# Optimization experiments

Hardware: AMD Instinct MI355X
Metric: run time of the kernel (lower is better)

The kernel has to match this reference:

```python
import jax, jax.numpy as jnp
import numpy as np

U, I, R, E, K, D, RD, OUT = 100000, 50000, 5, 100000, 4, 16, 64, 64
KF = 2      # selected factor index (self.k)
TAU = 0.5   # contrastive temperature


def setup_inputs() -> dict:
    key = jax.random.key(0)
    ks = jax.random.split(key, 17)
    inp = {
        'user_h': jax.random.normal(ks[0], (R, U, D), jnp.float32),
        'item_h': jax.random.normal(ks[1], (R, I, D), jnp.float32),
        'user_hsum': jax.random.normal(ks[2], (R, U, K, D), jnp.float32) * 0.25,
        'item_hsum': jax.random.normal(ks[3], (R, I, K, D), jnp.float32) * 0.25,
        'review_feat': jax.random.normal(ks[4], (R, E, K, RD), jnp.float32) * 0.2,
        'prototypes': jax.random.normal(ks[5], (K, RD), jnp.float32) * 0.2,
        'eta': jax.random.normal(ks[6], (R, E), jnp.float32),
        'node_w_fwd': jax.random.normal(ks[7], (R, D, D), jnp.float32) / np.sqrt(D),
        'node_w_rev': jax.random.normal(ks[8], (R, D, D), jnp.float32) / np.sqrt(D),
        'review_w_fwd': jax.random.normal(ks[9], (R, RD, D), jnp.float32) / np.sqrt(RD),
        'review_w_rev': jax.random.normal(ks[10], (R, RD, D), jnp.float32) / np.sqrt(RD),
        'ufc_w': jax.random.normal(ks[11], (D, OUT), jnp.float32) / np.sqrt(D),
        'ufc_b': jnp.zeros((OUT,), jnp.float32),
        'ifc_w': jax.random.normal(ks[12], (D, OUT), jnp.float32) / np.sqrt(D),
        'ifc_b': jnp.zeros((OUT,), jnp.float32),
        'rows': jax.random.randint(ks[13], (R, E), 0, U),
        'cols': jax.random.randint(ks[14], (R, E), 0, I),
    }
    return inp


def _l2n(x):
    return x / jnp.linalg.norm(x, axis=-1, keepdims=True)


def reference(user_h, item_h, user_hsum, item_hsum, review_feat, prototypes, eta,
              node_w_fwd, node_w_rev, review_w_fwd, review_w_rev,
              ufc_w, ufc_b, ifc_w, ifc_b, rows, cols):
    # --- per-rating contrastive edge scores (fwd and rev etypes are symmetric) ---
    ead_list = []
    norm_u = jnp.zeros((U,), user_h.dtype)
    norm_i = jnp.zeros((I,), user_h.dtype)
    for r in range(R):
        row, col = rows[r], cols[r]
        # factor-KF node similarity (L2-normalized feats)
        ru = _l2n(user_h[r])[row]               # [E, D]
        ri = _l2n(item_h[r])[col]               # [E, D]
        sim_k = jnp.sum(ru * ri, -1) / TAU      # [E]
        sim_all = jnp.sum(user_hsum[r][row] * item_hsum[r][col], -1) / TAU  # [E, K]
        exp_sim = jnp.exp(sim_k) / jnp.sum(jnp.exp(sim_all), -1)
        # prototype anchor scores on review features
        rf_k = review_feat[r, :, KF, :]                      # [E, RD]
        ad_k = (rf_k @ prototypes[KF]) / TAU                 # [E]
        ad_all = jnp.sum(review_feat[r] * prototypes, -1) / TAU  # [E, K]
        ead = jnp.exp(ad_k) / jnp.sum(jnp.exp(ad_all), -1)
        # sigmoid-gated combine with per-edge eta
        g = jax.nn.sigmoid(eta[r])
        ead = g * ead + (1.0 - g) * exp_sim
        ead_list.append(ead)
        # scatter-sum normalization; fwd+rev each contribute once, then /2 in torch
        norm_u = norm_u + jax.ops.segment_sum(ead, row, num_segments=U)
        norm_i = norm_i + jax.ops.segment_sum(ead, col, num_segments=I)
    # --- normalized edge weights + weighted message passing (HeteroGraphConv sum) ---
    ufeat = jnp.zeros((U, D), user_h.dtype)
    ifeat = jnp.zeros((I, D), user_h.dtype)
    int_dist = []
    for r in range(R):
        row, col = rows[r], cols[r]
        w = ead_list[r] / jnp.sqrt(norm_u[row] * norm_i[col])  # [E]
        int_dist.append(w[:, None])                            # item-side etype weights
        rf_k = review_feat[r, :, KF, :]
        # user -> item messages
        m_fwd = ((user_h[r] @ node_w_fwd[r])[row] + rf_k @ review_w_fwd[r]) * w[:, None]
        ifeat = ifeat + jax.ops.segment_sum(m_fwd, col, num_segments=I)
        # item -> user messages (rev etype, same review feats and weights)
        m_rev = ((item_h[r] @ node_w_rev[r])[col] + rf_k @ review_w_rev[r]) * w[:, None]
        ufeat = ufeat + jax.ops.segment_sum(m_rev, row, num_segments=U)
    int_dist = jnp.concatenate(int_dist, axis=0)  # [R*E, 1]
    leaky = lambda x: jnp.where(x >= 0, x, 0.1 * x)
    ufeat = leaky(ufeat) @ ufc_w + ufc_b
    ifeat = leaky(ifeat) @ ifc_w + ifc_b
    return ufeat, ifeat, int_dist
```

## Files before the change

kernel.cpp:

```cpp
#include <hip/hip_runtime.h>
#include <cstddef>

#define DEV_INLINE __device__ __forceinline__

constexpr int U_N = 100000;
constexpr int I_N = 50000;
constexpr int R_N = 5;
constexpr int E_N = 100000;
constexpr int K_N = 4;
constexpr int D_N = 16;
constexpr int RD_N = 64;
constexpr int OUT_N = 64;
constexpr int KF_N = 2;
constexpr float INV_TAU = 2.0f;

constexpr int NE_TOT = R_N * E_N;
constexpr int NNODE  = U_N + I_N;
constexpr int NB_SCAN = (NNODE + 255) / 256;

constexpr size_t OFS_CNT    = 0;
constexpr size_t OFS_OFF    = 150000;
constexpr size_t OFS_BSUMS  = 300016;
constexpr size_t OFS_CURSOR = 301040;
constexpr size_t OFS_LIST   = 451040;
constexpr size_t OFS_EAD    = 1451040;
constexpr size_t OFS_NORM   = 1951040;
constexpr size_t OFS_MFWD   = 2101040;
constexpr size_t OFS_MREV   = 10101040;

DEV_INLINE float dot4(float4 a, float4 b) { return a.x*b.x + a.y*b.y + a.z*b.z + a.w*b.w; }
DEV_INLINE void fma4(float4& a, float s, float4 w) { a.x += s*w.x; a.y += s*w.y; a.z += s*w.z; a.w += s*w.w; }
DEV_INLINE float comp(float4 v, int i) { return i == 0 ? v.x : i == 1 ? v.y : i == 2 ? v.z : v.w; }

__global__ __launch_bounds__(256) void count_kernel(
    const int* __restrict__ rows, const int* __restrict__ cols, int* __restrict__ cnt)
{
    const int idx = blockIdx.x * 256 + threadIdx.x;
    if (idx >= NE_TOT) return;
    atomicAdd(cnt + rows[idx], 1);
    atomicAdd(cnt + U_N + cols[idx], 1);
}

__global__ __launch_bounds__(256) void scan1_kernel(
    const int* __restrict__ cnt, int* __restrict__ off, int* __restrict__ bsums)
{
    __shared__ int s[256];
    const int t = threadIdx.x;
    const int i = blockIdx.x * 256 + t;
    const int v = (i < NNODE) ? cnt[i] : 0;
    s[t] = v;
    __syncthreads();
#pragma unroll
    for (int d = 1; d < 256; d <<= 1) {
        const int x = (t >= d) ? s[t - d] : 0;
        __syncthreads();
        s[t] += x;
        __syncthreads();
    }
    if (i < NNODE) off[i] = s[t] - v;
    if (t == 255) bsums[blockIdx.x] = s[255];
}

__global__ __launch_bounds__(1024) void scan2_kernel(int* __restrict__ bsums)
{
    __shared__ int s[1024];
    const int t = threadIdx.x;
    const int v = (t < NB_SCAN) ? bsums[t] : 0;
    s[t] = v;
    __syncthreads();
#pragma unroll
    for (int d = 1; d < 1024; d <<= 1) {
        const int x = (t >= d) ? s[t - d] : 0;
        __syncthreads();
        s[t] += x;
        __syncthreads();
    }
    if (t < NB_SCAN) bsums[t] = s[t] - v;
}

__global__ __launch_bounds__(256) void scan3_kernel(
    int* __restrict__ off, const int* __restrict__ bsums, int* __restrict__ cursor)
{
    const int i = blockIdx.x * 256 + threadIdx.x;
    if (i < NNODE) {
        const int v = off[i] + bsums[i >> 8];
        off[i] = v;
        cursor[i] = v;
    }
    if (i == 0) off[NNODE] = 2 * NE_TOT;
}

__global__ __launch_bounds__(256) void fill_kernel(
    const int* __restrict__ rows, const int* __restrict__ cols,
    int* __restrict__ cursor, int* __restrict__ list)
{
    const int idx = blockIdx.x * 256 + threadIdx.x;
    if (idx >= NE_TOT) return;
    const int p = atomicAdd(cursor + rows[idx], 1);
    list[p] = idx;
    const int q = atomicAdd(cursor + U_N + cols[idx], 1);
    list[q] = idx;
}

__global__ __launch_bounds__(256) void phase1_kernel(
    const float* __restrict__ user_h, const float* __restrict__ item_h,
    const float* __restrict__ user_hsum, const float* __restrict__ item_hsum,
    const float* __restrict__ review_feat, const float* __restrict__ prototypes,
    const float* __restrict__ eta,
    const float* __restrict__ node_w_fwd, const float* __restrict__ node_w_rev,
    const float* __restrict__ review_w_fwd, const float* __restrict__ review_w_rev,
    const int* __restrict__ rows, const int* __restrict__ cols,
    float* __restrict__ ead_ws,
    float* __restrict__ m_fwd, float* __restrict__ m_rev)
{
    __shared__ __align__(16) float proto_s[K_N * RD_N];
    __shared__ __align__(16) float nwf_s[D_N * D_N];
    __shared__ __align__(16) float nwr_s[D_N * D_N];
    __shared__ __align__(16) float rwf_s[RD_N * D_N];
    __shared__ __align__(16) float rwr_s[RD_N * D_N];
    const int tid = threadIdx.x;
    const int r = blockIdx.y;
    proto_s[tid] = prototypes[tid];
    nwf_s[tid] = node_w_fwd[r * D_N * D_N + tid];
    nwr_s[tid] = node_w_rev[r * D_N * D_N + tid];
#pragma unroll
    for (int q = 0; q < 4; ++q) {
        rwf_s[q*256 + tid] = review_w_fwd[r * RD_N * D_N + q*256 + tid];
        rwr_s[q*256 + tid] = review_w_rev[r * RD_N * D_N + q*256 + tid];
    }
    __syncthreads();

    const int e = blockIdx.x * 64 + (tid >> 2);
    const int l = tid & 3;
    if (e >= E_N) return;
    const size_t re = (size_t)r * E_N + e;
    const int row = rows[re];
    const int col = cols[re];

    const float4* uh4 = (const float4*)(user_h + ((size_t)r * U_N + row) * D_N);
    const float4* ih4 = (const float4*)(item_h + ((size_t)r * I_N + col) * D_N);
    const float4 a = uh4[l], b = ih4[l];
    float du = dot4(a, a), di = dot4(b, b), dui = dot4(a, b);
    du  += __shfl_xor(du, 1);  du  += __shfl_xor(du, 2);
    di  += __shfl_xor(di, 1);  di  += __shfl_xor(di, 2);
    dui += __shfl_xor(dui, 1); dui += __shfl_xor(dui, 2);
    const float sim_k = dui / sqrtf(du * di) * INV_TAU;

    const float4* us4 = (const float4*)(user_hsum + ((size_t)r * U_N + row) * (K_N * D_N)) + l * 4;
    const float4* is4 = (const float4*)(item_hsum + ((size_t)r * I_N + col) * (K_N * D_N)) + l * 4;
    float s = 0.f;
#pragma unroll
    for (int q = 0; q < 4; ++q) s += dot4(us4[q], is4[q]);
    float ssum = expf(s * INV_TAU);
    ssum += __shfl_xor(ssum, 1); ssum += __shfl_xor(ssum, 2);
    const float exp_sim = expf(sim_k) / ssum;

    const float4* rf4 = (const float4*)(review_feat + re * (size_t)(K_N * RD_N)) + l * 16;
    const float4* pr4 = (const float4*)proto_s + l * 16;
    float t = 0.f;
#pragma unroll
    for (int q = 0; q < 16; ++q) t += dot4(rf4[q], pr4[q]);
    t *= INV_TAU;
    float adsum = expf(t);
    adsum += __shfl_xor(adsum, 1); adsum += __shfl_xor(adsum, 2);
    const float adk = __shfl(t, KF_N, 4);
    const float ead_rev = expf(adk) / adsum;

    const float g = 1.0f / (1.0f + expf(-eta[re]));
    const float ead = g * ead_rev + (1.0f - g) * exp_sim;
    if (l == 0) ead_ws[re] = ead;

    float4 mf = make_float4(0.f, 0.f, 0.f, 0.f);
    float4 mr = make_float4(0.f, 0.f, 0.f, 0.f);
    const float4* nf4 = (const float4*)nwf_s;
    const float4* nr4 = (const float4*)nwr_s;
#pragma unroll
    for (int jq = 0; jq < 4; ++jq) {
        const float4 uv = uh4[jq];
        const float4 iv = ih4[jq];
#pragma unroll
        for (int jj = 0; jj < 4; ++jj) {
            const int j = jq*4 + jj;
            fma4(mf, comp(uv, jj), nf4[j*4 + l]);
            fma4(mr, comp(iv, jj), nr4[j*4 + l]);
        }
    }
    const float4* rfk4 = (const float4*)(review_feat + re * (size_t)(K_N * RD_N) + KF_N * RD_N);
    const float4* rf4w = (const float4*)rwf_s;
    const float4* rr4w = (const float4*)rwr_s;
#pragma unroll
    for (int jq = 0; jq < 16; ++jq) {
        const float4 v4 = rfk4[jq];
#pragma unroll
        for (int jj = 0; jj < 4; ++jj) {
            const int j = jq*4 + jj;
            fma4(mf, comp(v4, jj), rf4w[j*4 + l]);
            fma4(mr, comp(v4, jj), rr4w[j*4 + l]);
        }
    }
    *((float4*)(m_fwd + re * (size_t)D_N) + l) = mf;
    *((float4*)(m_rev + re * (size_t)D_N) + l) = mr;
}

__global__ __launch_bounds__(256) void norm_kernel(
    const int* __restrict__ off, const int* __restrict__ list,
    const float* __restrict__ ead, float* __restrict__ norm)
{
    const int n = blockIdx.x * 256 + threadIdx.x;
    if (n >= NNODE) return;
    const int p0 = off[n], p1 = off[n + 1];
    float acc = 0.f;
    for (int p = p0; p < p1; ++p) acc += ead[list[p]];
    norm[n] = acc;
}

__global__ __launch_bounds__(256) void wscale_kernel(
    const int* __restrict__ rows, const int* __restrict__ cols,
    const float* __restrict__ ead, const float* __restrict__ norm,
    float* __restrict__ w_out)
{
    const int idx = blockIdx.x * 256 + threadIdx.x;
    if (idx >= NE_TOT) return;
    const float nu = norm[rows[idx]];
    const float ni = norm[U_N + cols[idx]];
    w_out[idx] = ead[idx] / sqrtf(nu * ni);
}

__global__ __launch_bounds__(256) void gatherfc_kernel(
    const int* __restrict__ off, const int* __restrict__ list,
    const float* __restrict__ m_fwd, const float* __restrict__ m_rev,
    const float* __restrict__ w_edge,
    const float* __restrict__ ufc_w, const float* __restrict__ ufc_b,
    const float* __restrict__ ifc_w, const float* __restrict__ ifc_b,
    float* __restrict__ out)
{
    __shared__ __align__(16) float uw_s[D_N * OUT_N];
    __shared__ __align__(16) float iw_s[D_N * OUT_N];
    __shared__ __align__(16) float ub_s[OUT_N];
    __shared__ __align__(16) float ib_s[OUT_N];
    const int tid = threadIdx.x;
#pragma unroll
    for (int q = 0; q < 4; ++q) {
        uw_s[q*256 + tid] = ufc_w[q*256 + tid];
        iw_s[q*256 + tid] = ifc_w[q*256 + tid];
    }
    if (tid < OUT_N) ub_s[tid] = ufc_b[tid];
    else if (tid < 2*OUT_N) ib_s[tid - OUT_N] = ifc_b[tid - OUT_N];
    __syncthreads();

    const int gid = blockIdx.x * 256 + tid;
    const int n = gid >> 2;
    const int l = gid & 3;
    if (n >= NNODE) return;
    const int p0 = off[n], p1 = off[n + 1];
    const bool isU = (n < U_N);
    const float* __restrict__ src = isU ? m_rev : m_fwd;
    float4 acc = make_float4(0.f, 0.f, 0.f, 0.f);
    for (int p = p0; p < p1; ++p) {
        const int e = list[p];
        const float w = w_edge[e];
        const float4 v = *((const float4*)(src + (size_t)e * D_N) + l);
        fma4(acc, w, v);
    }
    acc.x = (acc.x >= 0.f) ? acc.x : 0.1f * acc.x;
    acc.y = (acc.y >= 0.f) ? acc.y : 0.1f * acc.y;
    acc.z = (acc.z >= 0.f) ? acc.z : 0.1f * acc.z;
    acc.w = (acc.w >= 0.f) ? acc.w : 0.1f * acc.w;

    const float* __restrict__ W = isU ? uw_s : iw_s;
    const float* __restrict__ B = isU ? ub_s : ib_s;
    float* __restrict__ dst = isU ? (out + (size_t)n * OUT_N)
                                  : (out + (size_t)U_N * OUT_N + (size_t)(n - U_N) * OUT_N);

    float4 s0 = *(const float4*)(B + 16*l + 0);
    float4 s1 = *(const float4*)(B + 16*l + 4);
    float4 s2 = *(const float4*)(B + 16*l + 8);
    float4 s3 = *(const float4*)(B + 16*l + 12);
#pragma unroll
    for (int sl = 0; sl < 4; ++sl) {
        float4 fv;
        fv.x = __shfl(acc.x, sl, 4);
        fv.y = __shfl(acc.y, sl, 4);
        fv.z = __shfl(acc.z, sl, 4);
        fv.w = __shfl(acc.w, sl, 4);
#pragma unroll
        for (int jj = 0; jj < 4; ++jj) {
            const int d = sl*4 + jj;
            const float x = comp(fv, jj);
            fma4(s0, x, *(const float4*)(W + d*OUT_N + 16*l + 0));
            fma4(s1, x, *(const float4*)(W + d*OUT_N + 16*l + 4));
            fma4(s2, x, *(const float4*)(W + d*OUT_N + 16*l + 8));
            fma4(s3, x, *(const float4*)(W + d*OUT_N + 16*l + 12));
        }
    }
    ((float4*)dst)[4*l + 0] = s0;
    ((float4*)dst)[4*l + 1] = s1;
    ((float4*)dst)[4*l + 2] = s2;
    ((float4*)dst)[4*l + 3] = s3;
}

extern "C" void kernel_launch(void* const* d_in, const int* in_sizes, int n_in,
                              void* d_out, int out_size, void* d_ws, size_t ws_size,
                              hipStream_t stream)
{
    const float* user_h       = (const float*)d_in[0];
    const float* item_h       = (const float*)d_in[1];
    const float* user_hsum    = (const float*)d_in[2];
    const float* item_hsum    = (const float*)d_in[3];
    const float* review_feat  = (const float*)d_in[4];
    const float* prototypes   = (const float*)d_in[5];
    const float* eta          = (const float*)d_in[6];
    const float* node_w_fwd   = (const float*)d_in[7];
    const float* node_w_rev   = (const float*)d_in[8];
    const float* review_w_fwd = (const float*)d_in[9];
    const float* review_w_rev = (const float*)d_in[10];
    const float* ufc_w        = (const float*)d_in[11];
    const float* ufc_b        = (const float*)d_in[12];
    const float* ifc_w        = (const float*)d_in[13];
    const float* ifc_b        = (const float*)d_in[14];
    const int*   rows         = (const int*)d_in[15];
    const int*   cols         = (const int*)d_in[16];

    int*   wsi = (int*)d_ws;
    float* wsf = (float*)d_ws;
    float* out = (float*)d_out;

    int*   cnt    = wsi + OFS_CNT;
    int*   off    = wsi + OFS_OFF;
    int*   bsums  = wsi + OFS_BSUMS;
    int*   cursor = wsi + OFS_CURSOR;
    int*   list   = wsi + OFS_LIST;
    float* ead    = wsf + OFS_EAD;
    float* norm   = wsf + OFS_NORM;
    float* m_fwd  = wsf + OFS_MFWD;
    float* m_rev  = wsf + OFS_MREV;

    hipMemsetAsync(cnt, 0, NNODE * sizeof(int), stream);

    const dim3 blk(256);
    const dim3 g_e((NE_TOT + 255) / 256);

    count_kernel<<<g_e, blk, 0, stream>>>(rows, cols, cnt);
    scan1_kernel<<<dim3(NB_SCAN), blk, 0, stream>>>(cnt, off, bsums);
    scan2_kernel<<<dim3(1), dim3(1024), 0, stream>>>(bsums);
    scan3_kernel<<<dim3((NNODE + 255) / 256), blk, 0, stream>>>(off, bsums, cursor);
    fill_kernel<<<g_e, blk, 0, stream>>>(rows, cols, cursor, list);

    phase1_kernel<<<dim3((E_N * 4 + 255) / 256, R_N), blk, 0, stream>>>(
        user_h, item_h, user_hsum, item_hsum, review_feat, prototypes, eta,
        node_w_fwd, node_w_rev, review_w_fwd, review_w_rev,
        rows, cols, ead, m_fwd, m_rev);

    norm_kernel<<<dim3((NNODE + 255) / 256), blk, 0, stream>>>(off, list, ead, norm);

    float* int_dist_out = out + (size_t)U_N * OUT_N + (size_t)I_N * OUT_N;
    wscale_kernel<<<g_e, blk, 0, stream>>>(rows, cols, ead, norm, int_dist_out);

    gatherfc_kernel<<<dim3((NNODE * 4 + 255) / 256), blk, 0, stream>>>(
        off, list, m_fwd, m_rev, int_dist_out,
        ufc_w, ufc_b, ifc_w, ifc_b, out);
}
```

Baseline: 1.083 ms.

## Fold degree counting and norm accumulation into phase1, replace scan with atomic allocation

```diff
diff --git a/kernel.cpp b/kernel.cpp
--- a/kernel.cpp
+++ b/kernel.cpp
@@ -16,91 +16,21 @@
 
 constexpr int NE_TOT = R_N * E_N;
 constexpr int NNODE  = U_N + I_N;
-constexpr int NB_SCAN = (NNODE + 255) / 256;
+constexpr int NB_ALLOC = (NNODE + 255) / 256;
 
 constexpr size_t OFS_CNT    = 0;
-constexpr size_t OFS_OFF    = 150000;
-constexpr size_t OFS_BSUMS  = 300016;
-constexpr size_t OFS_CURSOR = 301040;
-constexpr size_t OFS_LIST   = 451040;
-constexpr size_t OFS_EAD    = 1451040;
-constexpr size_t OFS_NORM   = 1951040;
-constexpr size_t OFS_MFWD   = 2101040;
-constexpr size_t OFS_MREV   = 10101040;
+constexpr size_t OFS_NORM   = 150000;
+constexpr size_t OFS_GCNT   = 300000;
+constexpr size_t OFS_OFF    = 300004;
+constexpr size_t OFS_CURSOR = 450004;
+constexpr size_t OFS_LIST   = 600004;
+constexpr size_t OFS_EAD    = 1600004;
+constexpr size_t OFS_MFWD   = 2100004;
+constexpr size_t OFS_MREV   = 10100004;
 
 DEV_INLINE float dot4(float4 a, float4 b) { return a.x*b.x + a.y*b.y + a.z*b.z + a.w*b.w; }
 DEV_INLINE void fma4(float4& a, float s, float4 w) { a.x += s*w.x; a.y += s*w.y; a.z += s*w.z; a.w += s*w.w; }
 DEV_INLINE float comp(float4 v, int i) { return i == 0 ? v.x : i == 1 ? v.y : i == 2 ? v.z : v.w; }
-
-__global__ __launch_bounds__(256) void count_kernel(
-    const int* __restrict__ rows, const int* __restrict__ cols, int* __restrict__ cnt)
-{
-    const int idx = blockIdx.x * 256 + threadIdx.x;
-    if (idx >= NE_TOT) return;
-    atomicAdd(cnt + rows[idx], 1);
-    atomicAdd(cnt + U_N + cols[idx], 1);
-}
-
-__global__ __launch_bounds__(256) void scan1_kernel(
-    const int* __restrict__ cnt, int* __restrict__ off, int* __restrict__ bsums)
-{
-    __shared__ int s[256];
-    const int t = threadIdx.x;
-    const int i = blockIdx.x * 256 + t;
-    const int v = (i < NNODE) ? cnt[i] : 0;
-    s[t] = v;
-    __syncthreads();
-#pragma unroll
-    for (int d = 1; d < 256; d <<= 1) {
-        const int x = (t >= d) ? s[t - d] : 0;
-        __syncthreads();
-        s[t] += x;
-        __syncthreads();
-    }
-    if (i < NNODE) off[i] = s[t] - v;
-    if (t == 255) bsums[blockIdx.x] = s[255];
-}
-
-__global__ __launch_bounds__(1024) void scan2_kernel(int* __restrict__ bsums)
-{
-    __shared__ int s[1024];
-    const int t = threadIdx.x;
-    const int v = (t < NB_SCAN) ? bsums[t] : 0;
-    s[t] = v;
-    __syncthreads();
-#pragma unroll
-    for (int d = 1; d < 1024; d <<= 1) {
-        const int x = (t >= d) ? s[t - d] : 0;
-        __syncthreads();
-        s[t] += x;
-        __syncthreads();
-    }
-    if (t < NB_SCAN) bsums[t] = s[t] - v;
-}
-
-__global__ __launch_bounds__(256) void scan3_kernel(
-    int* __restrict__ off, const int* __restrict__ bsums, int* __restrict__ cursor)
-{
-    const int i = blockIdx.x * 256 + threadIdx.x;
-    if (i < NNODE) {
-        const int v = off[i] + bsums[i >> 8];
-        off[i] = v;
-        cursor[i] = v;
-    }
-    if (i == 0) off[NNODE] = 2 * NE_TOT;
-}
-
-__global__ __launch_bounds__(256) void fill_kernel(
-    const int* __restrict__ rows, const int* __restrict__ cols,
-    int* __restrict__ cursor, int* __restrict__ list)
-{
-    const int idx = blockIdx.x * 256 + threadIdx.x;
-    if (idx >= NE_TOT) return;
-    const int p = atomicAdd(cursor + rows[idx], 1);
-    list[p] = idx;
-    const int q = atomicAdd(cursor + U_N + cols[idx], 1);
-    list[q] = idx;
-}
 
 __global__ __launch_bounds__(256) void phase1_kernel(
     const float* __restrict__ user_h, const float* __restrict__ item_h,
@@ -111,7 +41,8 @@
     const float* __restrict__ review_w_fwd, const float* __restrict__ review_w_rev,
     const int* __restrict__ rows, const int* __restrict__ cols,
     float* __restrict__ ead_ws,
-    float* __restrict__ m_fwd, float* __restrict__ m_rev)
+    float* __restrict__ m_fwd, float* __restrict__ m_rev,
+    int* __restrict__ cnt, float* __restrict__ norm)
 {
     __shared__ __align__(16) float proto_s[K_N * RD_N];
     __shared__ __align__(16) float nwf_s[D_N * D_N];
@@ -168,7 +99,13 @@
 
     const float g = 1.0f / (1.0f + expf(-eta[re]));
     const float ead = g * ead_rev + (1.0f - g) * exp_sim;
-    if (l == 0) ead_ws[re] = ead;
+    if (l == 0) {
+        ead_ws[re] = ead;
+        atomicAdd(cnt + row, 1);
+        atomicAdd(cnt + U_N + col, 1);
+        atomicAdd(norm + row, ead);
+        atomicAdd(norm + U_N + col, ead);
+    }
 
     float4 mf = make_float4(0.f, 0.f, 0.f, 0.f);
     float4 mr = make_float4(0.f, 0.f, 0.f, 0.f);
@@ -202,32 +139,60 @@
     *((float4*)(m_rev + re * (size_t)D_N) + l) = mr;
 }
 
-__global__ __launch_bounds__(256) void norm_kernel(
-    const int* __restrict__ off, const int* __restrict__ list,
-    const float* __restrict__ ead, float* __restrict__ norm)
-{
-    const int n = blockIdx.x * 256 + threadIdx.x;
-    if (n >= NNODE) return;
-    const int p0 = off[n], p1 = off[n + 1];
-    float acc = 0.f;
-    for (int p = p0; p < p1; ++p) acc += ead[list[p]];
-    norm[n] = acc;
-}
-
-__global__ __launch_bounds__(256) void wscale_kernel(
+__global__ __launch_bounds__(256) void alloc_kernel(
+    const int* __restrict__ cnt, int* __restrict__ off, int* __restrict__ cursor,
+    int* __restrict__ gcnt)
+{
+    __shared__ int s_wsum[4];
+    const int tid = threadIdx.x;
+    const int lane = tid & 63;
+    const int wid = tid >> 6;
+    const int n = blockIdx.x * 256 + tid;
+    const int v = (n < NNODE) ? cnt[n] : 0;
+    int incl = v;
+#pragma unroll
+    for (int d = 1; d < 64; d <<= 1) {
+        const int x = __shfl_up(incl, d);
+        if (lane >= d) incl += x;
+    }
+    if (lane == 63) s_wsum[wid] = incl;
+    __syncthreads();
+    if (tid == 0) {
+        const int t0 = s_wsum[0], t1 = s_wsum[1], t2 = s_wsum[2], t3 = s_wsum[3];
+        const int base = atomicAdd(gcnt, t0 + t1 + t2 + t3);
+        s_wsum[0] = base;
+        s_wsum[1] = base + t0;
+        s_wsum[2] = base + t0 + t1;
+        s_wsum[3] = base + t0 + t1 + t2;
+    }
+    __syncthreads();
+    if (n < NNODE) {
+        const int o = s_wsum[wid] + incl - v;
+        off[n] = o;
+        cursor[n] = o;
+    }
+}
+
+__global__ __launch_bounds__(256) void fillw_kernel(
     const int* __restrict__ rows, const int* __restrict__ cols,
     const float* __restrict__ ead, const float* __restrict__ norm,
+    int* __restrict__ cursor, int* __restrict__ list,
     float* __restrict__ w_out)
 {
     const int idx = blockIdx.x * 256 + threadIdx.x;
     if (idx >= NE_TOT) return;
-    const float nu = norm[rows[idx]];
-    const float ni = norm[U_N + cols[idx]];
-    w_out[idx] = ead[idx] / sqrtf(nu * ni);
+    const int row = rows[idx];
+    const int col = cols[idx];
+    const int p = atomicAdd(cursor + row, 1);
+    list[p] = idx;
+    const int q = atomicAdd(cursor + U_N + col, 1);
+    list[q] = idx;
+    w_out[idx] = ead[idx] / sqrtf(norm[row] * norm[U_N + col]);
 }
 
 __global__ __launch_bounds__(256) void gatherfc_kernel(
-    const int* __restrict__ off, const int* __restrict__ list,
+    const int* __restrict__ off, const int* __restrict__ cnt,
+    const int* __restrict__ list,
     const float* __restrict__ m_fwd, const float* __restrict__ m_rev,
     const float* __restrict__ w_edge,
     const float* __restrict__ ufc_w, const float* __restrict__ ufc_b,
@@ -252,7 +217,8 @@
     const int n = gid >> 2;
     const int l = gid & 3;
     if (n >= NNODE) return;
-    const int p0 = off[n], p1 = off[n + 1];
+    const int p0 = off[n];
+    const int p1 = p0 + cnt[n];
     const bool isU = (n < U_N);
     const float* __restrict__ src = isU ? m_rev : m_fwd;
     float4 acc = make_float4(0.f, 0.f, 0.f, 0.f);
@@ -326,37 +292,32 @@
     float* out = (float*)d_out;
 
     int*   cnt    = wsi + OFS_CNT;
+    float* norm   = wsf + OFS_NORM;
+    int*   gcnt   = wsi + OFS_GCNT;
     int*   off    = wsi + OFS_OFF;
-    int*   bsums  = wsi + OFS_BSUMS;
     int*   cursor = wsi + OFS_CURSOR;
     int*   list   = wsi + OFS_LIST;
     float* ead    = wsf + OFS_EAD;
-    float* norm   = wsf + OFS_NORM;
     float* m_fwd  = wsf + OFS_MFWD;
     float* m_rev  = wsf + OFS_MREV;
 
-    hipMemsetAsync(cnt, 0, NNODE * sizeof(int), stream);
+    hipMemsetAsync(wsi, 0, (2 * NNODE + 1) * sizeof(int), stream);
 
     const dim3 blk(256);
     const dim3 g_e((NE_TOT + 255) / 256);
-
-    count_kernel<<<g_e, blk, 0, stream>>>(rows, cols, cnt);
-    scan1_kernel<<<dim3(NB_SCAN), blk, 0, stream>>>(cnt, off, bsums);
-    scan2_kernel<<<dim3(1), dim3(1024), 0, stream>>>(bsums);
-    scan3_kernel<<<dim3((NNODE + 255) / 256), blk, 0, stream>>>(off, bsums, cursor);
-    fill_kernel<<<g_e, blk, 0, stream>>>(rows, cols, cursor, list);
 
     phase1_kernel<<<dim3((E_N * 4 + 255) / 256, R_N), blk, 0, stream>>>(
         user_h, item_h, user_hsum, item_hsum, review_feat, prototypes, eta,
         node_w_fwd, node_w_rev, review_w_fwd, review_w_rev,
-        rows, cols, ead, m_fwd, m_rev);
-
-    norm_kernel<<<dim3((NNODE + 255) / 256), blk, 0, stream>>>(off, list, ead, norm);
+        rows, cols, ead, m_fwd, m_rev, cnt, norm);
+
+    alloc_kernel<<<dim3(NB_ALLOC), blk, 0, stream>>>(cnt, off, cursor, gcnt);
 
     float* int_dist_out = out + (size_t)U_N * OUT_N + (size_t)I_N * OUT_N;
-    wscale_kernel<<<g_e, blk, 0, stream>>>(rows, cols, ead, norm, int_dist_out);
+    fillw_kernel<<<g_e, blk, 0, stream>>>(rows, cols, ead, norm, cursor, list,
+                                          int_dist_out);
 
     gatherfc_kernel<<<dim3((NNODE * 4 + 255) / 256), blk, 0, stream>>>(
-        off, list, m_fwd, m_rev, int_dist_out,
+        off, cnt, list, m_fwd, m_rev, int_dist_out,
         ufc_w, ufc_b, ifc_w, ifc_b, out);
 }
```

After: 1.054 ms. -2.7%, faster.
